# Optimization experiments

Hardware: AMD Instinct MI355X
Metric: run time of the kernel (lower is better)

## Reference

```python
import jax, jax.numpy as jnp
import numpy as np

B, S, DM, H = 2, 4096, 512, 8
DEPTH = DM // H


def setup_inputs() -> dict:
    key = jax.random.key(0)
    ks = jax.random.split(key, 12)
    scale = 1.0 / np.sqrt(DM)
    return {
        "q": jax.random.normal(ks[0], (B, S, DM), jnp.float32),
        "k": jax.random.normal(ks[1], (B, S, DM), jnp.float32),
        "v": jax.random.normal(ks[2], (B, S, DM), jnp.float32),
        # padding-style mask: 1.0 = masked position, 0.0 = attend
        "mask": jax.random.bernoulli(ks[3], 0.1, (B, 1, 1, S)).astype(jnp.float32),
        "Wq": jax.random.normal(ks[4], (DM, DM), jnp.float32) * scale,
        "bq": jnp.zeros((DM,), jnp.float32),
        "Wk": jax.random.normal(ks[5], (DM, DM), jnp.float32) * scale,
        "bk": jnp.zeros((DM,), jnp.float32),
        "Wv": jax.random.normal(ks[6], (DM, DM), jnp.float32) * scale,
        "bv": jnp.zeros((DM,), jnp.float32),
        "Wo": jax.random.normal(ks[7], (DM, DM), jnp.float32) * scale,
        "bo": jnp.zeros((DM,), jnp.float32),
    }


def _split_heads(x):
    # [B, S, DM] -> [B, H, S, DEPTH]
    b, s, _ = x.shape
    return x.reshape(b, s, H, DEPTH).transpose(0, 2, 1, 3)


def reference(q, k, v, mask, Wq, bq, Wk, bk, Wv, bv, Wo, bo):
    qh = _split_heads(q @ Wq + bq)   # [B,H,S,D]
    kh = _split_heads(k @ Wk + bk)
    vh = _split_heads(v @ Wv + bv)
    logits = jnp.einsum("bhqd,bhkd->bhqk", qh, kh) / jnp.sqrt(
        jnp.asarray(DEPTH, qh.dtype))
    logits = logits + mask * (-1e9)
    attn = jax.nn.softmax(logits, axis=-1)          # [B,H,Sq,Sk]
    out = jnp.einsum("bhqk,bhkd->bhqd", attn, vh)   # [B,H,S,D]
    out = out.transpose(0, 2, 1, 3).reshape(q.shape[0], -1, DM)
    return out @ Wo + bo
```

## Files before the change

kernel.cpp:

```cpp
#include <hip/hip_runtime.h>
#include <math.h>

#define BDIM 2
#define SDIM 4096
#define DMODEL 512
#define NHEAD 8
#define DHEAD 64
#define MROWS (BDIM * SDIM)

typedef __attribute__((ext_vector_type(8))) short short8;
typedef __attribute__((ext_vector_type(4))) float f32x4;

#define MFMA16(a, b, c) __builtin_amdgcn_mfma_f32_16x16x32_bf16((a), (b), (c), 0, 0, 0)
#define EXP2F(x) __builtin_amdgcn_exp2f(x)

#define SCALE2 0.18033688011112042f
#define MASKMUL -1.442695040e9f
#define M0C 16.0f

__device__ inline void bf16_split(float x, short& h, short& l) {
  unsigned u = __float_as_uint(x);
  h = (short)(u >> 16);
  float hf = __uint_as_float(u & 0xffff0000u);
  l = (short)(__float_as_uint(x - hf) >> 16);
}

__global__ __launch_bounds__(256) void wsplit_kernel(
    const float* __restrict__ W0, const float* __restrict__ W1,
    const float* __restrict__ W2, const float* __restrict__ W3,
    short* __restrict__ T0h, short* __restrict__ T0l, short* __restrict__ T1h,
    short* __restrict__ T1l, short* __restrict__ T2h, short* __restrict__ T2l,
    short* __restrict__ T3h, short* __restrict__ T3l) {
  __shared__ short Th[64 * 72], Tl[64 * 72];
  const int tid = threadIdx.x;
  const int k0 = blockIdx.x * 64;
  const int n0 = blockIdx.y * 64;
  const int z = blockIdx.z;
  const float* W = (z == 0) ? W0 : (z == 1) ? W1 : (z == 2) ? W2 : W3;
  short* Oh = (z == 0) ? T0h : (z == 1) ? T1h : (z == 2) ? T2h : T3h;
  short* Ol = (z == 0) ? T0l : (z == 1) ? T1l : (z == 2) ? T2l : T3l;

  {
    const int r = tid >> 2;
    const int c16 = (tid & 3) * 16;
    short8 h0, h1, l0, l1;
#pragma unroll
    for (int g = 0; g < 2; g++) {
      const f32x4 a = *(const f32x4*)(W + (size_t)(k0 + r) * DMODEL + n0 + c16 + g * 8);
      const f32x4 b = *(const f32x4*)(W + (size_t)(k0 + r) * DMODEL + n0 + c16 + g * 8 + 4);
      short8& hh = g ? h1 : h0;
      short8& ll = g ? l1 : l0;
#pragma unroll
      for (int j = 0; j < 4; j++) {
        short x, y;
        bf16_split(a[j], x, y);
        hh[j] = x;
        ll[j] = y;
        bf16_split(b[j], x, y);
        hh[4 + j] = x;
        ll[4 + j] = y;
      }
    }
    *(short8*)&Th[r * 72 + c16] = h0;
    *(short8*)&Th[r * 72 + c16 + 8] = h1;
    *(short8*)&Tl[r * 72 + c16] = l0;
    *(short8*)&Tl[r * 72 + c16 + 8] = l1;
  }
  __syncthreads();
  {
    const int n = tid >> 2;
    const int kc = (tid & 3) * 16;
    short8 h0, h1, l0, l1;
#pragma unroll
    for (int i = 0; i < 8; i++) {
      h0[i] = Th[(kc + i) * 72 + n];
      h1[i] = Th[(kc + 8 + i) * 72 + n];
      l0[i] = Tl[(kc + i) * 72 + n];
      l1[i] = Tl[(kc + 8 + i) * 72 + n];
    }
    short* dh = Oh + (size_t)(n0 + n) * DMODEL + k0 + kc;
    short* dl = Ol + (size_t)(n0 + n) * DMODEL + k0 + kc;
    *(short8*)dh = h0;
    *(short8*)(dh + 8) = h1;
    *(short8*)dl = l0;
    *(short8*)(dl + 8) = l1;
  }
}

template <int MODE>
__global__ __launch_bounds__(256, 4) void proj_mfma_kernel(
    const float* __restrict__ X, const short* __restrict__ Wth,
    const short* __restrict__ Wtl, const float* __restrict__ bias,
    float* __restrict__ out, short* __restrict__ oh, short* __restrict__ ol) {
  __shared__ short Xh[64 * 72], Xl[64 * 72];
  __shared__ short Wh[64 * 72], Wl[64 * 72];

  const int tid = threadIdx.x;
  const int lane = tid & 63;
  const int w = tid >> 6;
  const int lane15 = lane & 15;
  const int quad = lane >> 4;
  const int wm = (w >> 1) * 32;
  const int wn = (w & 1) * 32;
  const int m0 = blockIdx.x * 64;
  const int n0 = blockIdx.y * 64;

  f32x4 c[2][2];
#pragma unroll
  for (int mt = 0; mt < 2; mt++)
#pragma unroll
    for (int nt = 0; nt < 2; nt++) c[mt][nt] = (f32x4){0.f, 0.f, 0.f, 0.f};

  const int sr = tid >> 2;
  const int sc16 = (tid & 3) * 16;

  for (int k0 = 0; k0 < DMODEL; k0 += 64) {
    {
      short8 h0, h1, l0, l1;
#pragma unroll
      for (int g = 0; g < 2; g++) {
        const f32x4 a =
            *(const f32x4*)(X + (size_t)(m0 + sr) * DMODEL + k0 + sc16 + g * 8);
        const f32x4 b = *(const f32x4*)(X + (size_t)(m0 + sr) * DMODEL + k0 +
                                        sc16 + g * 8 + 4);
        short8& hh = g ? h1 : h0;
        short8& ll = g ? l1 : l0;
#pragma unroll
        for (int j = 0; j < 4; j++) {
          short x, y;
          bf16_split(a[j], x, y);
          hh[j] = x;
          ll[j] = y;
          bf16_split(b[j], x, y);
          hh[4 + j] = x;
          ll[4 + j] = y;
        }
      }
      *(short8*)&Xh[sr * 72 + sc16] = h0;
      *(short8*)&Xh[sr * 72 + sc16 + 8] = h1;
      *(short8*)&Xl[sr * 72 + sc16] = l0;
      *(short8*)&Xl[sr * 72 + sc16 + 8] = l1;

      const short* wsh = Wth + (size_t)(n0 + sr) * DMODEL + k0 + sc16;
      const short* wsl = Wtl + (size_t)(n0 + sr) * DMODEL + k0 + sc16;
      *(short8*)&Wh[sr * 72 + sc16] = *(const short8*)wsh;
      *(short8*)&Wh[sr * 72 + sc16 + 8] = *(const short8*)(wsh + 8);
      *(short8*)&Wl[sr * 72 + sc16] = *(const short8*)wsl;
      *(short8*)&Wl[sr * 72 + sc16 + 8] = *(const short8*)(wsl + 8);
    }
    __syncthreads();

#pragma unroll
    for (int ks = 0; ks < 2; ks++) {
      short8 ah[2], al[2], bh[2], bl[2];
#pragma unroll
      for (int mt = 0; mt < 2; mt++) {
        const int xo = (wm + mt * 16 + lane15) * 72 + ks * 32 + quad * 8;
        ah[mt] = *(const short8*)&Xh[xo];
        al[mt] = *(const short8*)&Xl[xo];
      }
#pragma unroll
      for (int nt = 0; nt < 2; nt++) {
        const int wo = (wn + nt * 16 + lane15) * 72 + ks * 32 + quad * 8;
        bh[nt] = *(const short8*)&Wh[wo];
        bl[nt] = *(const short8*)&Wl[wo];
      }
#pragma unroll
      for (int mt = 0; mt < 2; mt++)
#pragma unroll
        for (int nt = 0; nt < 2; nt++) {
          c[mt][nt] = MFMA16(ah[mt], bh[nt], c[mt][nt]);
          c[mt][nt] = MFMA16(ah[mt], bl[nt], c[mt][nt]);
          c[mt][nt] = MFMA16(al[mt], bh[nt], c[mt][nt]);
        }
    }
    __syncthreads();
  }

#pragma unroll
  for (int nt = 0; nt < 2; nt++) {
    const int n = n0 + wn + nt * 16 + lane15;
    const float bb = bias[n];
#pragma unroll
    for (int mt = 0; mt < 2; mt++)
#pragma unroll
      for (int r = 0; r < 4; r++) {
        const int m = m0 + wm + mt * 16 + quad * 4 + r;
        const float val = c[mt][nt][r] + bb;
        if (MODE == 1) {
          const int bidx = m >> 12;
          const int s = m & 4095;
          const int hh = n >> 6;
          const int d = n & 63;
          const size_t off =
              ((size_t)(bidx * NHEAD + hh) * SDIM + s) * DHEAD + d;
          short x, y;
          bf16_split(val, x, y);
          oh[off] = x;
          ol[off] = y;
        } else {
          out[(size_t)m * DMODEL + n] = val;
        }
      }
  }
}

__global__ __launch_bounds__(256) void vtrans_kernel(
    const short* __restrict__ vh, const short* __restrict__ vl,
    short* __restrict__ vth, short* __restrict__ vtl) {
  __shared__ short Th[64 * 72], Tl[64 * 72];
  const int tid = threadIdx.x;
  const int s0 = blockIdx.x * 64;
  const int h = blockIdx.y;
  const int b = blockIdx.z;
  const size_t base = (size_t)(b * NHEAD + h) * SDIM * DHEAD;

  {
    const int s = tid >> 2;
    const int c = tid & 3;
    const short* srcH = vh + base + (size_t)(s0 + s) * DHEAD + c * 16;
    const short* srcL = vl + base + (size_t)(s0 + s) * DHEAD + c * 16;
    *(short8*)&Th[s * 72 + c * 16] = *(const short8*)srcH;
    *(short8*)&Th[s * 72 + c * 16 + 8] = *(const short8*)(srcH + 8);
    *(short8*)&Tl[s * 72 + c * 16] = *(const short8*)srcL;
    *(short8*)&Tl[s * 72 + c * 16 + 8] = *(const short8*)(srcL + 8);
  }
  __syncthreads();
  {
    const int d = tid & 63;
    const int cw = tid >> 6;
    short8 a0, a1, b0, b1;
#pragma unroll
    for (int i = 0; i < 8; i++) {
      a0[i] = Th[(cw * 16 + i) * 72 + d];
      a1[i] = Th[(cw * 16 + 8 + i) * 72 + d];
      b0[i] = Tl[(cw * 16 + i) * 72 + d];
      b1[i] = Tl[(cw * 16 + 8 + i) * 72 + d];
    }
    short* dstH = vth + base + (size_t)d * SDIM + s0 + cw * 16;
    short* dstL = vtl + base + (size_t)d * SDIM + s0 + cw * 16;
    *(short8*)dstH = a0;
    *(short8*)(dstH + 8) = a1;
    *(short8*)dstL = b0;
    *(short8*)(dstL + 8) = b1;
  }
}

#define KP 72
#define VP 72
#define PP 68

__global__ __launch_bounds__(256, 2) void flash_attn_kernel(
    const short* __restrict__ qhh, const short* __restrict__ qhl,
    const short* __restrict__ khh, const short* __restrict__ khl,
    const short* __restrict__ vth, const short* __restrict__ vtl,
    const float* __restrict__ mask, float* __restrict__ ctx) {
  __shared__ short Ksh[64 * KP], Ksl[64 * KP];
  __shared__ short Vsh[64 * VP], Vsl[64 * VP];
  __shared__ float Ps[128 * PP];

  const int tid = threadIdx.x;
  const int lane = tid & 63;
  const int w = tid >> 6;
  const int lane15 = lane & 15;
  const int quad = lane >> 4;
  const int q0 = blockIdx.x * 128;
  const int h = blockIdx.y;
  const int b = blockIdx.z;

  const size_t base = (size_t)(b * NHEAD + h) * SDIM * DHEAD;
  const short* Qh = qhh + base;
  const short* Ql = qhl + base;
  const short* Kh = khh + base;
  const short* Kl = khl + base;
  const short* Vh = vth + base;
  const short* Vl = vtl + base;
  const float* mb = mask + (size_t)b * SDIM;

  short8 qfh[2][2], qfl[2][2];
#pragma unroll
  for (int mt = 0; mt < 2; mt++) {
    const size_t row = q0 + w * 32 + mt * 16 + lane15;
#pragma unroll
    for (int ks = 0; ks < 2; ks++) {
      qfh[mt][ks] = *(const short8*)(Qh + row * DHEAD + ks * 32 + quad * 8);
      qfl[mt][ks] = *(const short8*)(Ql + row * DHEAD + ks * 32 + quad * 8);
    }
  }

  f32x4 o[2][4];
#pragma unroll
  for (int mt = 0; mt < 2; mt++)
#pragma unroll
    for (int dt = 0; dt < 4; dt++) o[mt][dt] = (f32x4){0.f, 0.f, 0.f, 0.f};
  float lr[2][4];
#pragma unroll
  for (int mt = 0; mt < 2; mt++)
#pragma unroll
    for (int r = 0; r < 4; r++) lr[mt][r] = 0.f;

  short8 onesb;
#pragma unroll
  for (int j = 0; j < 8; j++) onesb[j] = (short)0x3F80;

  const int sr = tid >> 2;
  const int sc = (tid & 3) * 16;

  for (int kt = 0; kt < SDIM / 64; kt++) {
    const int k0 = kt * 64;
    {
      const short8 a0 = *(const short8*)(Kh + (size_t)(k0 + sr) * DHEAD + sc);
      const short8 a1 = *(const short8*)(Kh + (size_t)(k0 + sr) * DHEAD + sc + 8);
      const short8 b0 = *(const short8*)(Kl + (size_t)(k0 + sr) * DHEAD + sc);
      const short8 b1 = *(const short8*)(Kl + (size_t)(k0 + sr) * DHEAD + sc + 8);
      const short8 c0 = *(const short8*)(Vh + (size_t)sr * SDIM + k0 + sc);
      const short8 c1 = *(const short8*)(Vh + (size_t)sr * SDIM + k0 + sc + 8);
      const short8 d0 = *(const short8*)(Vl + (size_t)sr * SDIM + k0 + sc);
      const short8 d1 = *(const short8*)(Vl + (size_t)sr * SDIM + k0 + sc + 8);
      *(short8*)&Ksh[sr * KP + sc] = a0;
      *(short8*)&Ksh[sr * KP + sc + 8] = a1;
      *(short8*)&Ksl[sr * KP + sc] = b0;
      *(short8*)&Ksl[sr * KP + sc + 8] = b1;
      *(short8*)&Vsh[sr * VP + sc] = c0;
      *(short8*)&Vsh[sr * VP + sc + 8] = c1;
      *(short8*)&Vsl[sr * VP + sc] = d0;
      *(short8*)&Vsl[sr * VP + sc + 8] = d1;
    }
    float mv[4];
#pragma unroll
    for (int nt = 0; nt < 4; nt++)
      mv[nt] = fmaf(mb[k0 + nt * 16 + lane15], MASKMUL, -M0C);
    __syncthreads();

#pragma unroll
    for (int mt = 0; mt < 2; mt++)
#pragma unroll
      for (int nt = 0; nt < 4; nt++) {
        f32x4 acc = (f32x4){0.f, 0.f, 0.f, 0.f};
#pragma unroll
        for (int ks = 0; ks < 2; ks++) {
          const int koff = (nt * 16 + lane15) * KP + ks * 32 + quad * 8;
          const short8 kbh = *(const short8*)&Ksh[koff];
          const short8 kbl = *(const short8*)&Ksl[koff];
          acc = MFMA16(qfh[mt][ks], kbh, acc);
          acc = MFMA16(qfh[mt][ks], kbl, acc);
          acc = MFMA16(qfl[mt][ks], kbh, acc);
        }
#pragma unroll
        for (int r = 0; r < 4; r++) {
          const float p = EXP2F(fmaf(acc[r], SCALE2, mv[nt]));
          Ps[(w * 32 + mt * 16 + quad * 4 + r) * PP + nt * 16 + lane15] = p;
        }
      }

    short8 pah[2][2], pal[2][2];
#pragma unroll
    for (int mt = 0; mt < 2; mt++)
#pragma unroll
      for (int kf = 0; kf < 2; kf++) {
        const float* pr =
            &Ps[(w * 32 + mt * 16 + lane15) * PP + kf * 32 + quad * 8];
        const f32x4 p0 = *(const f32x4*)pr;
        const f32x4 p1 = *(const f32x4*)(pr + 4);
        short8 ph, pl;
#pragma unroll
        for (int j = 0; j < 4; j++) {
          short hh, ll;
          bf16_split(p0[j], hh, ll);
          ph[j] = hh;
          pl[j] = ll;
        }
#pragma unroll
        for (int j = 0; j < 4; j++) {
          short hh, ll;
          bf16_split(p1[j], hh, ll);
          ph[4 + j] = hh;
          pl[4 + j] = ll;
        }
        pah[mt][kf] = ph;
        pal[mt][kf] = pl;
      }

#pragma unroll
    for (int mt = 0; mt < 2; mt++) {
      f32x4 racc = (f32x4){0.f, 0.f, 0.f, 0.f};
#pragma unroll
      for (int kf = 0; kf < 2; kf++) {
        racc = MFMA16(pah[mt][kf], onesb, racc);
        racc = MFMA16(pal[mt][kf], onesb, racc);
      }
#pragma unroll
      for (int r = 0; r < 4; r++) lr[mt][r] += racc[r];
    }

#pragma unroll
    for (int dt = 0; dt < 4; dt++)
#pragma unroll
      for (int kf = 0; kf < 2; kf++) {
        const int voff = (dt * 16 + lane15) * VP + kf * 32 + quad * 8;
        const short8 vbh = *(const short8*)&Vsh[voff];
        const short8 vbl = *(const short8*)&Vsl[voff];
#pragma unroll
        for (int mt = 0; mt < 2; mt++) {
          o[mt][dt] = MFMA16(pah[mt][kf], vbh, o[mt][dt]);
          o[mt][dt] = MFMA16(pah[mt][kf], vbl, o[mt][dt]);
          o[mt][dt] = MFMA16(pal[mt][kf], vbh, o[mt][dt]);
        }
      }
    __syncthreads();
  }

  float inv[2][4];
#pragma unroll
  for (int mt = 0; mt < 2; mt++)
#pragma unroll
    for (int r = 0; r < 4; r++) inv[mt][r] = 1.f / lr[mt][r];
#pragma unroll
  for (int mt = 0; mt < 2; mt++)
#pragma unroll
    for (int dt = 0; dt < 4; dt++)
#pragma unroll
      for (int r = 0; r < 4; r++) {
        const int q = q0 + w * 32 + mt * 16 + quad * 4 + r;
        const int col = h * DHEAD + dt * 16 + lane15;
        ctx[((size_t)b * SDIM + q) * DMODEL + col] = o[mt][dt][r] * inv[mt][r];
      }
}

extern "C" void kernel_launch(void* const* d_in, const int* in_sizes, int n_in,
                              void* d_out, int out_size, void* d_ws,
                              size_t ws_size, hipStream_t stream) {
  const float* q = (const float*)d_in[0];
  const float* k = (const float*)d_in[1];
  const float* v = (const float*)d_in[2];
  const float* mask = (const float*)d_in[3];
  const float* Wq = (const float*)d_in[4];
  const float* bq = (const float*)d_in[5];
  const float* Wk = (const float*)d_in[6];
  const float* bk = (const float*)d_in[7];
  const float* Wv = (const float*)d_in[8];
  const float* bv = (const float*)d_in[9];
  const float* Wo = (const float*)d_in[10];
  const float* bo = (const float*)d_in[11];
  float* out = (float*)d_out;

  char* W = (char*)d_ws;
  const size_t SZB = (size_t)MROWS * DMODEL * sizeof(short);
  short* q_h = (short*)(W + 0 * SZB);
  short* q_l = (short*)(W + 1 * SZB);
  short* k_h = (short*)(W + 2 * SZB);
  short* k_l = (short*)(W + 3 * SZB);
  short* v_h = (short*)(W + 4 * SZB);
  short* v_l = (short*)(W + 5 * SZB);
  short* vt_h = (short*)(W + 6 * SZB);
  short* vt_l = (short*)(W + 7 * SZB);
  float* ctx = (float*)(W + 4 * SZB);
  const size_t WSZ = (size_t)DMODEL * DMODEL * sizeof(short);
  char* WT = W + 8 * SZB;
  short* wtq_h = (short*)(WT + 0 * WSZ);
  short* wtq_l = (short*)(WT + 1 * WSZ);
  short* wtk_h = (short*)(WT + 2 * WSZ);
  short* wtk_l = (short*)(WT + 3 * WSZ);
  short* wtv_h = (short*)(WT + 4 * WSZ);
  short* wtv_l = (short*)(WT + 5 * WSZ);
  short* wto_h = (short*)(WT + 6 * WSZ);
  short* wto_l = (short*)(WT + 7 * WSZ);

  wsplit_kernel<<<dim3(DMODEL / 64, DMODEL / 64, 4), 256, 0, stream>>>(
      Wq, Wk, Wv, Wo, wtq_h, wtq_l, wtk_h, wtk_l, wtv_h, wtv_l, wto_h, wto_l);

  const dim3 gproj(MROWS / 64, DMODEL / 64);
  proj_mfma_kernel<1><<<gproj, 256, 0, stream>>>(q, wtq_h, wtq_l, bq, nullptr,
                                                 q_h, q_l);
  proj_mfma_kernel<1><<<gproj, 256, 0, stream>>>(k, wtk_h, wtk_l, bk, nullptr,
                                                 k_h, k_l);
  proj_mfma_kernel<1><<<gproj, 256, 0, stream>>>(v, wtv_h, wtv_l, bv, nullptr,
                                                 v_h, v_l);

  vtrans_kernel<<<dim3(SDIM / 64, NHEAD, BDIM), 256, 0, stream>>>(v_h, v_l,
                                                                  vt_h, vt_l);

  flash_attn_kernel<<<dim3(SDIM / 128, NHEAD, BDIM), 256, 0, stream>>>(
      q_h, q_l, k_h, k_l, vt_h, vt_l, mask, ctx);

  proj_mfma_kernel<0><<<gproj, 256, 0, stream>>>(ctx, wto_h, wto_l, bo, out,
                                                 nullptr, nullptr);
}
```

Before: 405.6 us.

## Switch flash attention to 32x32x16 MFMA tiles and pre-split P into packed bf16

The attention kernel now uses 32x32x16 bf16 MFMA instructions instead of 16x16x32, so each wave covers its 32 query rows with a single tile, and the fragment layout changes to match. The exp'd probabilities are split into hi/lo bf16 when they are written and stored packed as one int in shared memory. The read side then only unpacks, instead of reloading floats and splitting them. Larger MFMA tiles cut the instruction count and LDS fragment reloads, but they use more accumulator registers, which may affect occupancy with the 2-blocks launch bound.

```diff
diff --git a/kernel.cpp b/kernel.cpp
--- a/kernel.cpp
+++ b/kernel.cpp
@@ -10,8 +10,11 @@
 
 typedef __attribute__((ext_vector_type(8))) short short8;
 typedef __attribute__((ext_vector_type(4))) float f32x4;
+typedef __attribute__((ext_vector_type(16))) float f32x16;
+typedef __attribute__((ext_vector_type(4))) int i32x4;
 
 #define MFMA16(a, b, c) __builtin_amdgcn_mfma_f32_16x16x32_bf16((a), (b), (c), 0, 0, 0)
+#define MFMA32(a, b, c) __builtin_amdgcn_mfma_f32_32x32x16_bf16((a), (b), (c), 0, 0, 0)
 #define EXP2F(x) __builtin_amdgcn_exp2f(x)
 
 #define SCALE2 0.18033688011112042f
@@ -257,13 +260,13 @@
     const float* __restrict__ mask, float* __restrict__ ctx) {
   __shared__ short Ksh[64 * KP], Ksl[64 * KP];
   __shared__ short Vsh[64 * VP], Vsl[64 * VP];
-  __shared__ float Ps[128 * PP];
+  __shared__ int Ps[128 * PP];
 
   const int tid = threadIdx.x;
   const int lane = tid & 63;
   const int w = tid >> 6;
-  const int lane15 = lane & 15;
-  const int quad = lane >> 4;
+  const int l31 = lane & 31;
+  const int half = lane >> 5;
   const int q0 = blockIdx.x * 128;
   const int h = blockIdx.y;
   const int b = blockIdx.z;
@@ -277,27 +280,23 @@
   const short* Vl = vtl + base;
   const float* mb = mask + (size_t)b * SDIM;
 
-  short8 qfh[2][2], qfl[2][2];
-#pragma unroll
-  for (int mt = 0; mt < 2; mt++) {
-    const size_t row = q0 + w * 32 + mt * 16 + lane15;
-#pragma unroll
-    for (int ks = 0; ks < 2; ks++) {
-      qfh[mt][ks] = *(const short8*)(Qh + row * DHEAD + ks * 32 + quad * 8);
-      qfl[mt][ks] = *(const short8*)(Ql + row * DHEAD + ks * 32 + quad * 8);
-    }
-  }
-
-  f32x4 o[2][4];
-#pragma unroll
-  for (int mt = 0; mt < 2; mt++)
-#pragma unroll
-    for (int dt = 0; dt < 4; dt++) o[mt][dt] = (f32x4){0.f, 0.f, 0.f, 0.f};
-  float lr[2][4];
-#pragma unroll
-  for (int mt = 0; mt < 2; mt++)
-#pragma unroll
-    for (int r = 0; r < 4; r++) lr[mt][r] = 0.f;
+  short8 qfh[4], qfl[4];
+  {
+    const size_t row = q0 + w * 32 + l31;
+#pragma unroll
+    for (int c = 0; c < 4; c++) {
+      qfh[c] = *(const short8*)(Qh + row * DHEAD + c * 16 + half * 8);
+      qfl[c] = *(const short8*)(Ql + row * DHEAD + c * 16 + half * 8);
+    }
+  }
+
+  f32x16 o[2], lsum;
+#pragma unroll
+  for (int i = 0; i < 16; i++) {
+    o[0][i] = 0.f;
+    o[1][i] = 0.f;
+    lsum[i] = 0.f;
+  }
 
   short8 onesb;
 #pragma unroll
@@ -326,105 +325,87 @@
       *(short8*)&Vsl[sr * VP + sc] = d0;
       *(short8*)&Vsl[sr * VP + sc + 8] = d1;
     }
-    float mv[4];
-#pragma unroll
-    for (int nt = 0; nt < 4; nt++)
-      mv[nt] = fmaf(mb[k0 + nt * 16 + lane15], MASKMUL, -M0C);
+    float mv[2];
+#pragma unroll
+    for (int t = 0; t < 2; t++)
+      mv[t] = fmaf(mb[k0 + t * 32 + l31], MASKMUL, -M0C);
     __syncthreads();
 
 #pragma unroll
-    for (int mt = 0; mt < 2; mt++)
-#pragma unroll
-      for (int nt = 0; nt < 4; nt++) {
-        f32x4 acc = (f32x4){0.f, 0.f, 0.f, 0.f};
-#pragma unroll
-        for (int ks = 0; ks < 2; ks++) {
-          const int koff = (nt * 16 + lane15) * KP + ks * 32 + quad * 8;
-          const short8 kbh = *(const short8*)&Ksh[koff];
-          const short8 kbl = *(const short8*)&Ksl[koff];
-          acc = MFMA16(qfh[mt][ks], kbh, acc);
-          acc = MFMA16(qfh[mt][ks], kbl, acc);
-          acc = MFMA16(qfl[mt][ks], kbh, acc);
-        }
-#pragma unroll
-        for (int r = 0; r < 4; r++) {
-          const float p = EXP2F(fmaf(acc[r], SCALE2, mv[nt]));
-          Ps[(w * 32 + mt * 16 + quad * 4 + r) * PP + nt * 16 + lane15] = p;
-        }
-      }
-
-    short8 pah[2][2], pal[2][2];
-#pragma unroll
-    for (int mt = 0; mt < 2; mt++)
-#pragma unroll
-      for (int kf = 0; kf < 2; kf++) {
-        const float* pr =
-            &Ps[(w * 32 + mt * 16 + lane15) * PP + kf * 32 + quad * 8];
-        const f32x4 p0 = *(const f32x4*)pr;
-        const f32x4 p1 = *(const f32x4*)(pr + 4);
-        short8 ph, pl;
-#pragma unroll
-        for (int j = 0; j < 4; j++) {
-          short hh, ll;
-          bf16_split(p0[j], hh, ll);
-          ph[j] = hh;
-          pl[j] = ll;
-        }
-#pragma unroll
-        for (int j = 0; j < 4; j++) {
-          short hh, ll;
-          bf16_split(p1[j], hh, ll);
-          ph[4 + j] = hh;
-          pl[4 + j] = ll;
-        }
-        pah[mt][kf] = ph;
-        pal[mt][kf] = pl;
-      }
-
-#pragma unroll
-    for (int mt = 0; mt < 2; mt++) {
-      f32x4 racc = (f32x4){0.f, 0.f, 0.f, 0.f};
-#pragma unroll
-      for (int kf = 0; kf < 2; kf++) {
-        racc = MFMA16(pah[mt][kf], onesb, racc);
-        racc = MFMA16(pal[mt][kf], onesb, racc);
-      }
-#pragma unroll
-      for (int r = 0; r < 4; r++) lr[mt][r] += racc[r];
-    }
-
-#pragma unroll
-    for (int dt = 0; dt < 4; dt++)
-#pragma unroll
-      for (int kf = 0; kf < 2; kf++) {
-        const int voff = (dt * 16 + lane15) * VP + kf * 32 + quad * 8;
+    for (int t = 0; t < 2; t++) {
+      f32x16 acc;
+#pragma unroll
+      for (int i = 0; i < 16; i++) acc[i] = 0.f;
+#pragma unroll
+      for (int c = 0; c < 4; c++) {
+        const int koff = (t * 32 + l31) * KP + c * 16 + half * 8;
+        const short8 kbh = *(const short8*)&Ksh[koff];
+        const short8 kbl = *(const short8*)&Ksl[koff];
+        acc = MFMA32(qfh[c], kbh, acc);
+        acc = MFMA32(qfh[c], kbl, acc);
+        acc = MFMA32(qfl[c], kbh, acc);
+      }
+#pragma unroll
+      for (int reg = 0; reg < 16; reg++) {
+        const int row = (reg & 3) + 8 * (reg >> 2) + 4 * half;
+        const float p = EXP2F(fmaf(acc[reg], SCALE2, mv[t]));
+        short ph, pl;
+        bf16_split(p, ph, pl);
+        Ps[(w * 32 + row) * PP + t * 32 + l31] =
+            (((int)(unsigned short)ph) << 16) | (int)(unsigned short)pl;
+      }
+    }
+
+    short8 pah[4], pal[4];
+#pragma unroll
+    for (int kc = 0; kc < 4; kc++) {
+      const int* pr = &Ps[(w * 32 + l31) * PP + kc * 16 + half * 8];
+      const i32x4 w0 = *(const i32x4*)pr;
+      const i32x4 w1 = *(const i32x4*)(pr + 4);
+      short8 ph, pl;
+#pragma unroll
+      for (int j = 0; j < 4; j++) {
+        ph[j] = (short)((unsigned)w0[j] >> 16);
+        pl[j] = (short)(w0[j] & 0xffff);
+        ph[4 + j] = (short)((unsigned)w1[j] >> 16);
+        pl[4 + j] = (short)(w1[j] & 0xffff);
+      }
+      pah[kc] = ph;
+      pal[kc] = pl;
+    }
+
+#pragma unroll
+    for (int kc = 0; kc < 4; kc++) {
+      lsum = MFMA32(pah[kc], onesb, lsum);
+      lsum = MFMA32(pal[kc], onesb, lsum);
+    }
+
+#pragma unroll
+    for (int t2 = 0; t2 < 2; t2++)
+#pragma unroll
+      for (int kc = 0; kc < 4; kc++) {
+        const int voff = (t2 * 32 + l31) * VP + kc * 16 + half * 8;
         const short8 vbh = *(const short8*)&Vsh[voff];
         const short8 vbl = *(const short8*)&Vsl[voff];
-#pragma unroll
-        for (int mt = 0; mt < 2; mt++) {
-          o[mt][dt] = MFMA16(pah[mt][kf], vbh, o[mt][dt]);
-          o[mt][dt] = MFMA16(pah[mt][kf], vbl, o[mt][dt]);
-          o[mt][dt] = MFMA16(pal[mt][kf], vbh, o[mt][dt]);
-        }
+        o[t2] = MFMA32(pah[kc], vbh, o[t2]);
+        o[t2] = MFMA32(pah[kc], vbl, o[t2]);
+        o[t2] = MFMA32(pal[kc], vbh, o[t2]);
       }
     __syncthreads();
   }
 
-  float inv[2][4];
-#pragma unroll
-  for (int mt = 0; mt < 2; mt++)
-#pragma unroll
-    for (int r = 0; r < 4; r++) inv[mt][r] = 1.f / lr[mt][r];
-#pragma unroll
-  for (int mt = 0; mt < 2; mt++)
-#pragma unroll
-    for (int dt = 0; dt < 4; dt++)
-#pragma unroll
-      for (int r = 0; r < 4; r++) {
-        const int q = q0 + w * 32 + mt * 16 + quad * 4 + r;
-        const int col = h * DHEAD + dt * 16 + lane15;
-        ctx[((size_t)b * SDIM + q) * DMODEL + col] = o[mt][dt][r] * inv[mt][r];
-      }
+  float inv[16];
+#pragma unroll
+  for (int reg = 0; reg < 16; reg++) inv[reg] = 1.f / lsum[reg];
+#pragma unroll
+  for (int t2 = 0; t2 < 2; t2++)
+#pragma unroll
+    for (int reg = 0; reg < 16; reg++) {
+      const int q = q0 + w * 32 + (reg & 3) + 8 * (reg >> 2) + 4 * half;
+      const int d = t2 * 32 + l31;
+      ctx[((size_t)b * SDIM + q) * DMODEL + h * DHEAD + d] =
+          o[t2][reg] * inv[reg];
+    }
 }
 
 extern "C" void kernel_launch(void* const* d_in, const int* in_sizes, int n_in,
@@ -455,6 +436,7 @@
   short* vt_h = (short*)(W + 6 * SZB);
   short* vt_l = (short*)(W + 7 * SZB);
   float* ctx = (float*)(W + 4 * SZB);
+
   const size_t WSZ = (size_t)DMODEL * DMODEL * sizeof(short);
   char* WT = W + 8 * SZB;
   short* wtq_h = (short*)(WT + 0 * WSZ);
```

Measured after the change: 407.5 us. Within noise of the previous version (+0.5%).
